# Kernel tuning notes

Hardware: AMD Instinct MI355X
Metric: run time of the kernel (lower is better)

## Reference

```python
import jax, jax.numpy as jnp
import numpy as np

N, DIM, HEADS, DH, WS = 32768, 1024, 8, 64, 256
INNER = HEADS * DH
MASK_VAL = -1e10  # ATTN_MASK_VALUE
EPS = 1e-5


def setup_inputs() -> dict:
    key = jax.random.key(0)
    k0, k1, k2 = jax.random.split(key, 3)
    x = jax.random.normal(k0, (N, DIM), jnp.float32)
    # rotary sin/cos with interleaved-pair layout matching rotate_every_two
    inv_freq = 1.0 / (10000.0 ** (jnp.arange(0, DH, 2, dtype=jnp.float32) / DH))
    freqs = jnp.arange(N, dtype=jnp.float32)[:, None] * inv_freq[None, :]  # [N, DH/2]
    sin = jnp.repeat(jnp.sin(freqs), 2, axis=-1)  # [N, DH]
    cos = jnp.repeat(jnp.cos(freqs), 2, axis=-1)  # [N, DH]
    gamma = jnp.ones((DIM,), jnp.float32)
    beta = jnp.zeros((DIM,), jnp.float32)
    w_qkv = jax.random.normal(k1, (DIM, 3 * INNER), jnp.float32) * 0.02
    w_out = jax.random.normal(k2, (INNER, DIM), jnp.float32) * 0.02
    b_out = jnp.zeros((DIM,), jnp.float32)
    return dict(x=x, sin=sin, cos=cos, gamma=gamma, beta=beta,
                w_qkv=w_qkv, w_out=w_out, b_out=b_out)


def _rotate_every_two(t):
    t1, t2 = t[..., 0::2], t[..., 1::2]
    return jnp.stack((-t2, t1), axis=-1).reshape(t.shape)


def _apply_rotary(t, sin, cos):
    # rot_dim == DH (full rotary), so no pass-through slice needed
    return t * cos + _rotate_every_two(t) * sin


def reference(x, sin, cos, gamma, beta, w_qkv, w_out, b_out):
    # LayerNorm (elementwise affine)
    mu = jnp.mean(x, axis=-1, keepdims=True)
    var = jnp.var(x, axis=-1, keepdims=True)
    x = (x - mu) * jax.lax.rsqrt(var + EPS) * gamma + beta
    # token shift: shift first half of channels by one token
    half = DIM // 2
    x_shift = jnp.pad(x[:, :half], ((1, 0), (0, 0)))[:-1]
    x = jnp.concatenate([x_shift, x[:, half:]], axis=-1)
    # qkv projection (no bias)
    qkv = x @ w_qkv  # [N, 3*INNER]
    q, k, v = jnp.split(qkv, 3, axis=-1)
    to_heads = lambda t: t.reshape(N, HEADS, DH).transpose(1, 0, 2)  # [H, N, DH]
    q, k, v = to_heads(q), to_heads(k), to_heads(v)
    # inline rotary on q, k AND v (as in source)
    q = _apply_rotary(q, sin, cos)
    k = _apply_rotary(k, sin, cos)
    v = _apply_rotary(v, sin, cos)
    # window split: [H, w, WS, DH]
    w = N // WS
    q, k, v = (t.reshape(HEADS, w, WS, DH) for t in (q, k, v))
    # look-back: each window attends to (previous window ++ current window)
    def lookback(t):
        t = jnp.pad(t, ((0, 0), (1, 0), (0, 0), (0, 0)))  # zero window at front
        return jnp.concatenate([t[:, :-1], t[:, 1:]], axis=2)  # [H, w, 2*WS, DH]
    k, v = lookback(k), lookback(v)
    sim = jnp.einsum('hwid,hwjd->hwij', q, k) * (DH ** -0.5)  # [H, w, WS, 2*WS]
    mask = jnp.tril(jnp.ones((WS, 2 * WS), dtype=bool), k=WS)  # j <= i + WS (causal)
    sim = jnp.where(mask, sim, MASK_VAL)
    attn = jax.nn.softmax(sim, axis=-1)
    out = jnp.einsum('hwij,hwjd->hwid', attn, v)  # [H, w, WS, DH]
    out = out.transpose(1, 2, 0, 3).reshape(N, INNER)  # '(w n) (h d)'
    return out @ w_out + b_out
```

## Files before the change

kernel.cpp:

```cpp
#include <hip/hip_runtime.h>

typedef __attribute__((ext_vector_type(4))) unsigned short us4;
typedef __attribute__((ext_vector_type(8))) unsigned short us8;
typedef __attribute__((ext_vector_type(8))) short s8;
typedef __attribute__((ext_vector_type(4))) float f32x4;
typedef __attribute__((ext_vector_type(16))) float f32x16;

#define NTOK 32768
#define DIM_ 1024
#define HEADS_ 8
#define DH_ 64
#define WS_ 256
#define NWIN_ 128
#define INNER_ 512

__device__ __forceinline__ float b2f(unsigned short u) {
  union { unsigned u; float f; } x; x.u = ((unsigned)u) << 16; return x.f;
}
__device__ __forceinline__ unsigned short f2b(float f) {
  union { float f; unsigned u; } x; x.f = f;
  unsigned r = x.u + 0x7FFFu + ((x.u >> 16) & 1u);
  return (unsigned short)(r >> 16);
}
__device__ __forceinline__ unsigned pk2(float a, float b) {
  return (unsigned)f2b(a) | ((unsigned)f2b(b) << 16);
}
__device__ __forceinline__ s8 mk_s8(unsigned w0, unsigned w1, unsigned w2, unsigned w3) {
  union { unsigned u[4]; s8 v; } x;
  x.u[0] = w0; x.u[1] = w1; x.u[2] = w2; x.u[3] = w3;
  return x.v;
}

__device__ __forceinline__ void gload_lds16(const unsigned short* g, void* l) {
  __builtin_amdgcn_global_load_lds((const __attribute__((address_space(1))) void*)g,
                                   (__attribute__((address_space(3))) void*)l, 16, 0, 0);
}

__global__ __launch_bounds__(256) void ln_shift(const float* __restrict__ x,
                                                const float* __restrict__ gamma,
                                                const float* __restrict__ beta,
                                                unsigned short* __restrict__ xs) {
  int row = blockIdx.x;
  int t = threadIdx.x;
  f32x4 v = ((const f32x4*)(x + (size_t)row * DIM_))[t];
  float sum = 0.f, ss = 0.f;
#pragma unroll
  for (int j = 0; j < 4; j++) { sum += v[j]; ss += v[j] * v[j]; }
#pragma unroll
  for (int off = 32; off >= 1; off >>= 1) {
    sum += __shfl_xor(sum, off);
    ss  += __shfl_xor(ss, off);
  }
  __shared__ float red[2][4];
  int wave = t >> 6, l = t & 63;
  if (l == 0) { red[0][wave] = sum; red[1][wave] = ss; }
  __syncthreads();
  sum = red[0][0] + red[0][1] + red[0][2] + red[0][3];
  ss  = red[1][0] + red[1][1] + red[1][2] + red[1][3];
  float mu = sum * (1.0f / DIM_);
  float var = ss * (1.0f / DIM_) - mu * mu;
  float rs = rsqrtf(var + 1e-5f);
  f32x4 g = ((const f32x4*)gamma)[t];
  f32x4 bb = ((const f32x4*)beta)[t];
  us4 o;
#pragma unroll
  for (int j = 0; j < 4; j++) o[j] = f2b((v[j] - mu) * rs * g[j] + bb[j]);
  int c0 = t * 4;
  if (c0 >= 512) {
    *(us4*)(xs + (size_t)row * DIM_ + c0) = o;
  } else {
    if (row + 1 < NTOK) *(us4*)(xs + (size_t)(row + 1) * DIM_ + c0) = o;
    if (row == 0) { us4 z = {0, 0, 0, 0}; *(us4*)(xs + c0) = z; }
  }
}

__global__ __launch_bounds__(256) void transpose_f32_bf16(const float* __restrict__ in,
                                                          unsigned short* __restrict__ out,
                                                          int R, int C) {
  __shared__ unsigned short tile[32][33];
  int bx = blockIdx.x * 32, by = blockIdx.y * 32;
  int tx = threadIdx.x, ty = threadIdx.y;
#pragma unroll
  for (int i = 0; i < 32; i += 8) tile[ty + i][tx] = f2b(in[(size_t)(by + ty + i) * C + bx + tx]);
  __syncthreads();
#pragma unroll
  for (int i = 0; i < 32; i += 8) out[(size_t)(bx + ty + i) * R + by + tx] = tile[tx][ty + i];
}

template <int MODE>
__global__ __launch_bounds__(512, 2) void gemm_p12(const unsigned short* __restrict__ A,
                                                   const unsigned short* __restrict__ Bt,
                                                   void* __restrict__ Cv,
                                                   const float* __restrict__ bias,
                                                   const float* __restrict__ sinp,
                                                   const float* __restrict__ cosp,
                                                   unsigned short* __restrict__ qh,
                                                   unsigned short* __restrict__ kh,
                                                   unsigned short* __restrict__ vt,
                                                   int M, int N, int K) {
  __shared__ __align__(16) char lds[163840];
  int t = threadIdx.x;
  int l = t & 63, lg = l >> 4, ll = l & 15;
  int wave = t >> 6;
  int wm = wave >> 2, wn = wave & 3;

  int nbx = gridDim.x;
  int nwg = nbx * gridDim.y;
  int flat = blockIdx.y * nbx + blockIdx.x;
  int swz = (flat & 7) * (nwg >> 3) + (flat >> 3);
  int m0 = (swz / nbx) * 256, n0 = (swz % nbx) * 256;

  const f32x4 fz = {0.f, 0.f, 0.f, 0.f};
  f32x4 acc[8][4];
#pragma unroll
  for (int m = 0; m < 8; m++)
#pragma unroll
    for (int n = 0; n < 4; n++) acc[m][n] = fz;

  int srow = t >> 3;
  int sunit = (t & 7) ^ (srow & 7);
  const unsigned short* gA = A + (size_t)(m0 + srow) * K + sunit * 8;
  const unsigned short* gB = Bt + (size_t)(n0 + srow) * K + sunit * 8;
  int t16 = t * 16;
  int nk = K >> 6;

#pragma unroll
  for (int j = 0; j < 4; j++) gload_lds16(gA + (size_t)(j * 64) * K, lds + j * 8192 + t16);
#pragma unroll
  for (int j = 0; j < 4; j++) gload_lds16(gB + (size_t)(j * 64) * K, lds + 98304 + j * 8192 + t16);
#pragma unroll
  for (int j = 0; j < 4; j++) gload_lds16(gA + 64 + (size_t)(j * 64) * K, lds + 32768 + j * 8192 + t16);
  asm volatile("s_waitcnt vmcnt(4)" ::: "memory");
  __builtin_amdgcn_sched_barrier(0);
  __builtin_amdgcn_s_barrier();

  for (int kt = 0; kt < nk; ++kt) {
    const char* sa = lds + (kt % 3) * 32768;
    const char* sb = lds + 98304 + (kt & 1) * 32768;
    s8 bf[4];
#pragma unroll
    for (int p = 0; p < 4; ++p) {
      const int qm = p & 1, kk = p >> 1;
      __builtin_amdgcn_sched_barrier(0);
      s8 af[4];
#pragma unroll
      for (int m = 0; m < 4; m++) {
        int r = wm * 128 + qm * 64 + m * 16 + ll;
        af[m] = *(const s8*)(sa + r * 128 + (((kk * 4 + lg) ^ (r & 7)) << 4));
      }
      if (qm == 0) {
#pragma unroll
        for (int n = 0; n < 4; n++) {
          int r = wn * 64 + n * 16 + ll;
          bf[n] = *(const s8*)(sb + r * 128 + (((kk * 4 + lg) ^ (r & 7)) << 4));
        }
      }
      if (p == 0 && kt + 1 < nk) {
        const unsigned short* nB = gB + (kt + 1) * 64;
        char* dB = lds + 98304 + ((kt + 1) & 1) * 32768;
#pragma unroll
        for (int j = 0; j < 4; j++) gload_lds16(nB + (size_t)(j * 64) * K, dB + j * 8192 + t16);
      }
      if (p == 1 && kt + 2 < nk) {
        const unsigned short* nA = gA + (kt + 2) * 64;
        char* dA = lds + ((kt + 2) % 3) * 32768;
#pragma unroll
        for (int j = 0; j < 4; j++) gload_lds16(nA + (size_t)(j * 64) * K, dA + j * 8192 + t16);
      }
      __builtin_amdgcn_sched_barrier(0);
      __builtin_amdgcn_s_barrier();
      __builtin_amdgcn_sched_barrier(0);
      __builtin_amdgcn_s_setprio(1);
#pragma unroll
      for (int m = 0; m < 4; m++)
#pragma unroll
        for (int n = 0; n < 4; n++)
          acc[qm * 4 + m][n] =
              __builtin_amdgcn_mfma_f32_16x16x32_bf16(af[m], bf[n], acc[qm * 4 + m][n], 0, 0, 0);
      __builtin_amdgcn_s_setprio(0);
      if (p == 3) {
        if (kt < nk - 2)       asm volatile("s_waitcnt vmcnt(4)" ::: "memory");
        else if (kt == nk - 2) asm volatile("s_waitcnt vmcnt(0)" ::: "memory");
      }
      __builtin_amdgcn_sched_barrier(0);
      __builtin_amdgcn_s_barrier();
    }
  }

  if (MODE == 0) {
    int third = n0 >> 9;
    if (third == 2) {
      bool odd = (ll & 1) != 0;
#pragma unroll
      for (int m = 0; m < 8; m++) {
        int row0 = m0 + wm * 128 + m * 16 + lg * 4;
#pragma unroll
        for (int n = 0; n < 4; n++) {
          int cit = (n0 - 1024) + wn * 64 + n * 16 + ll;
          int head = cit >> 6, d = cit & 63;
          us4 st;
#pragma unroll
          for (int r = 0; r < 4; r++) {
            float v = acc[m][n][r];
            float p = __shfl_xor(v, 1);
            float sn = sinp[(size_t)(row0 + r) * 64 + d];
            float cs = cosp[(size_t)(row0 + r) * 64 + d];
            st[r] = f2b(odd ? (v * cs + p * sn) : (v * cs - p * sn));
          }
          *(us4*)(vt + ((size_t)head * 64 + d) * NTOK + row0) = st;
        }
      }
    } else {
      int b = ll & 3, q = ll >> 2;
      bool bo1 = (b & 1) != 0, bo2 = (b & 2) != 0;
#pragma unroll
      for (int m = 0; m < 8; m++) {
        int row = m0 + wm * 128 + m * 16 + lg * 4 + b;
#pragma unroll
        for (int n = 0; n < 4; n++) {
          float v0 = acc[m][n][0], v1 = acc[m][n][1], v2 = acc[m][n][2], v3 = acc[m][n][3];
          float x0 = __shfl_xor(v1, 1);
          float x1 = __shfl_xor(v0, 1);
          float x2 = __shfl_xor(v3, 1);
          float x3 = __shfl_xor(v2, 1);
          float u0 = bo1 ? x0 : v0;
          float u1 = bo1 ? v1 : x1;
          float u2 = bo1 ? x2 : v2;
          float u3 = bo1 ? v3 : x3;
          float y0 = __shfl_xor(u2, 2);
          float y1 = __shfl_xor(u3, 2);
          float y2 = __shfl_xor(u0, 2);
          float y3 = __shfl_xor(u1, 2);
          float w0 = bo2 ? y0 : u0;
          float w1 = bo2 ? y1 : u1;
          float w2 = bo2 ? u2 : y2;
          float w3 = bo2 ? u3 : y3;
          int cb = n0 + wn * 64 + n * 16 + q * 4;
          int cit = cb & 511;
          int head = cit >> 6, d0 = cit & 63;
          f32x4 s4 = *(const f32x4*)(sinp + (size_t)row * 64 + d0);
          f32x4 c4 = *(const f32x4*)(cosp + (size_t)row * 64 + d0);
          us4 st;
          st[0] = f2b(w0 * c4[0] - w1 * s4[0]);
          st[1] = f2b(w1 * c4[1] + w0 * s4[1]);
          st[2] = f2b(w2 * c4[2] - w3 * s4[2]);
          st[3] = f2b(w3 * c4[3] + w2 * s4[3]);
          if (third == 0) *(us4*)(qh + ((size_t)head * NTOK + row) * 64 + d0) = st;
          else            *(us4*)(kh + ((size_t)head * NTOK + row) * 64 + d0) = st;
        }
      }
    }
  } else {
#pragma unroll
    for (int n = 0; n < 4; n++) {
      int col = n0 + wn * 64 + n * 16 + ll;
      float bs = bias ? bias[col] : 0.0f;
#pragma unroll
      for (int m = 0; m < 8; m++) {
#pragma unroll
        for (int r = 0; r < 4; r++) {
          int row = m0 + wm * 128 + m * 16 + lg * 4 + r;
          ((float*)Cv)[(size_t)row * N + col] = acc[m][n][r] + bs;
        }
      }
    }
  }
}

__global__ __launch_bounds__(256, 4) void attn_kernel(const unsigned short* __restrict__ qh,
                                                      const unsigned short* __restrict__ kh,
                                                      const unsigned short* __restrict__ vt,
                                                      unsigned short* __restrict__ ao) {
  __shared__ char kbuf[2][8192];
  __shared__ char vbuf[8192];
  int half = blockIdx.x, w = blockIdx.y, h = blockIdx.z;
  int t = threadIdx.x;
  int wave = t >> 6, l = t & 63;
  int l31 = l & 31, hi = l >> 5;
  const unsigned short* qb = qh + (size_t)h * NTOK * 64;
  const unsigned short* kb = kh + (size_t)h * NTOK * 64;
  const unsigned short* vb = vt + (size_t)h * 64 * NTOK;

  int qw = half * 128 + wave * 32 + l31;
  int qn = w * 256 + qw;
  s8 qf[4];
#pragma unroll
  for (int dht = 0; dht < 4; dht++)
    qf[dht] = *(const s8*)(qb + (size_t)qn * 64 + dht * 16 + hi * 8);

  f32x16 o0 = {}, o1 = {};
  float dsum = (w == 0) ? 128.f : 0.f;
  int n0 = w * 256 - 256;
  int c0 = (w == 0) ? 4 : 0;

  int srow = wave * 16 + (l >> 3);
  int sunit = l & 7;

  {
    const unsigned short* g = kb + (size_t)(n0 + c0 * 64 + srow) * 64 + ((sunit ^ (srow & 7)) * 8);
    gload_lds16(g, kbuf[c0 & 1] + wave * 2048);
    gload_lds16(g + 8 * 64, kbuf[c0 & 1] + wave * 2048 + 1024);
  }
  __syncthreads();

  for (int c = c0; c < 8; ++c) {
    int cb = n0 + c * 64;
    {
      int d = srow;
      const unsigned short* g = vb + (size_t)d * NTOK + cb + ((sunit ^ (d & 7)) * 8);
      gload_lds16(g, vbuf + wave * 2048);
      gload_lds16(g + (size_t)8 * NTOK, vbuf + wave * 2048 + 1024);
    }
    if (c < 7) {
      const unsigned short* g = kb + (size_t)(cb + 64 + srow) * 64 + ((sunit ^ (srow & 7)) * 8);
      gload_lds16(g, kbuf[(c + 1) & 1] + wave * 2048);
      gload_lds16(g + 8 * 64, kbuf[(c + 1) & 1] + wave * 2048 + 1024);
    }

    f32x16 s[2] = {{}, {}};
    const char* kl = kbuf[c & 1];
#pragma unroll
    for (int kt = 0; kt < 2; kt++) {
#pragma unroll
      for (int dht = 0; dht < 4; dht++) {
        int row = kt * 32 + l31;
        int unit = (dht * 2 + hi) ^ (row & 7);
        s8 kf = *(const s8*)(kl + row * 128 + unit * 16);
        s[kt] = __builtin_amdgcn_mfma_f32_32x32x16_bf16(kf, qf[dht], s[kt], 0, 0, 0);
      }
    }

    unsigned P0[2][4], P1[2][4];
#pragma unroll
    for (int kt = 0; kt < 2; kt++) {
#pragma unroll
      for (int r = 0; r < 16; r++) {
        int j = c * 64 + kt * 32 + (r & 3) + 8 * (r >> 2) + hi * 4;
        float e = (j <= qw + 256) ? __expf(s[kt][r] * 0.125f) : 0.f;
        s[kt][r] = e;
        dsum += e;
      }
#pragma unroll
      for (int j2 = 0; j2 < 4; j2++) {
        P0[kt][j2] = pk2(s[kt][j2 * 4 + 0], s[kt][j2 * 4 + 1]);
        P1[kt][j2] = pk2(s[kt][j2 * 4 + 2], s[kt][j2 * 4 + 3]);
      }
    }

    __syncthreads();

#pragma unroll
    for (int tt = 0; tt < 4; tt++) {
      int kt = tt >> 1, ss = tt & 1;
      unsigned a = P0[kt][2 * ss], b = P1[kt][2 * ss];
      unsigned cx = P0[kt][2 * ss + 1], dx = P1[kt][2 * ss + 1];
      asm volatile("v_permlane32_swap_b32 %0, %1" : "+v"(a), "+v"(cx));
      asm volatile("v_permlane32_swap_b32 %0, %1" : "+v"(b), "+v"(dx));
      s8 pf = mk_s8(a, b, cx, dx);
      {
        int row = l31;
        int unit = (tt * 2 + hi) ^ (row & 7);
        s8 vf = *(const s8*)(vbuf + row * 128 + unit * 16);
        o0 = __builtin_amdgcn_mfma_f32_32x32x16_bf16(vf, pf, o0, 0, 0, 0);
      }
      {
        int row = 32 + l31;
        int unit = (tt * 2 + hi) ^ (row & 7);
        s8 vf = *(const s8*)(vbuf + row * 128 + unit * 16);
        o1 = __builtin_amdgcn_mfma_f32_32x32x16_bf16(vf, pf, o1, 0, 0, 0);
      }
    }
    __syncthreads();
  }

  dsum += __shfl_xor(dsum, 32);
  float inv = 1.f / dsum;

  unsigned short* orow = ao + (size_t)qn * INNER_ + h * 64;
#pragma unroll
  for (int g = 0; g < 4; g++) {
    us4 st0, st1;
#pragma unroll
    for (int rr = 0; rr < 4; rr++) {
      st0[rr] = f2b(o0[g * 4 + rr] * inv);
      st1[rr] = f2b(o1[g * 4 + rr] * inv);
    }
    *(us4*)(orow + g * 8 + hi * 4) = st0;
    *(us4*)(orow + 32 + g * 8 + hi * 4) = st1;
  }
}

extern "C" void kernel_launch(void* const* d_in, const int* in_sizes, int n_in,
                              void* d_out, int out_size, void* d_ws, size_t ws_size,
                              hipStream_t stream) {
  const float* x     = (const float*)d_in[0];
  const float* sin_  = (const float*)d_in[1];
  const float* cos_  = (const float*)d_in[2];
  const float* gamma = (const float*)d_in[3];
  const float* beta  = (const float*)d_in[4];
  const float* w_qkv = (const float*)d_in[5];
  const float* w_out = (const float*)d_in[6];
  const float* b_out = (const float*)d_in[7];

  char* ws = (char*)d_ws;
  const size_t OFF_WQT = 0;
  const size_t OFF_WOT = 3145728;
  const size_t OFF_XS  = 4194304;
  const size_t OFF_QH  = 71303168;
  const size_t OFF_KH  = 104857600;
  const size_t OFF_VT  = 138412032;
  const size_t NEEDED  = 171966464;
  if (ws_size < NEEDED) return;

  unsigned short* wqT = (unsigned short*)(ws + OFF_WQT);
  unsigned short* woT = (unsigned short*)(ws + OFF_WOT);
  unsigned short* xs  = (unsigned short*)(ws + OFF_XS);
  unsigned short* qh  = (unsigned short*)(ws + OFF_QH);
  unsigned short* kh  = (unsigned short*)(ws + OFF_KH);
  unsigned short* vt  = (unsigned short*)(ws + OFF_VT);
  unsigned short* ao  = xs;

  transpose_f32_bf16<<<dim3(1536 / 32, 1024 / 32), dim3(32, 8), 0, stream>>>(w_qkv, wqT, 1024, 1536);
  transpose_f32_bf16<<<dim3(1024 / 32, 512 / 32), dim3(32, 8), 0, stream>>>(w_out, woT, 512, 1024);
  ln_shift<<<NTOK, 256, 0, stream>>>(x, gamma, beta, xs);
  gemm_p12<0><<<dim3(1536 / 256, NTOK / 256), 512, 0, stream>>>(
      xs, wqT, nullptr, nullptr, sin_, cos_, qh, kh, vt, NTOK, 1536, 1024);
  attn_kernel<<<dim3(2, NWIN_, HEADS_), 256, 0, stream>>>(qh, kh, vt, ao);
  gemm_p12<1><<<dim3(1024 / 256, NTOK / 256), 512, 0, stream>>>(
      ao, woT, (void*)d_out, b_out, nullptr, nullptr, nullptr, nullptr, nullptr, NTOK, 1024, 512);
}
```

Before: 334.0 us.

## Load GEMM B operand directly into registers, double-buffer A in LDS

Reworks the bf16 GEMM main loop so the weight (B) fragments are loaded from global memory straight into registers with register double-buffering, instead of staging them through LDS. The A tile uses a two-stage LDS double buffer in place of the previous three-stage one, which cuts LDS to 64 KB and the number of barriers per k-step. The trade-off is more VGPR use for the B fragments, direct global loads per wave that may be less coalesced and are duplicated across waves sharing wn, and a full vmcnt(0) wait at the end of each k-step, which may expose load latency.

```diff
diff --git a/kernel.cpp b/kernel.cpp
--- a/kernel.cpp
+++ b/kernel.cpp
@@ -87,8 +87,56 @@
   for (int i = 0; i < 32; i += 8) out[(size_t)(bx + ty + i) * R + by + tx] = tile[tx][ty + i];
 }
 
+__device__ __forceinline__ void gemm_tile_body(int kt, int nk, char* lds,
+                                               const unsigned short* gA,
+                                               const unsigned short* gB0,
+                                               const unsigned short* gB1,
+                                               const unsigned short* gB2,
+                                               const unsigned short* gB3,
+                                               int K, int t16,
+                                               f32x4 (&acc)[8][4],
+                                               s8 (&bu)[8], s8 (&bn)[8],
+                                               int wm, int ll, int lg) {
+  const char* sa = lds + (kt & 1) * 32768;
+  __builtin_amdgcn_sched_barrier(0);
+  if (kt + 1 < nk) {
+    char* dA = lds + ((kt + 1) & 1) * 32768;
+    const unsigned short* nA = gA + (kt + 1) * 64;
+#pragma unroll
+    for (int j = 0; j < 4; j++) gload_lds16(nA + (size_t)(j * 64) * K, dA + j * 8192 + t16);
+    int c = (kt + 1) * 64;
+    bn[0] = *(const s8*)(gB0 + c);  bn[4] = *(const s8*)(gB0 + c + 32);
+    bn[1] = *(const s8*)(gB1 + c);  bn[5] = *(const s8*)(gB1 + c + 32);
+    bn[2] = *(const s8*)(gB2 + c);  bn[6] = *(const s8*)(gB2 + c + 32);
+    bn[3] = *(const s8*)(gB3 + c);  bn[7] = *(const s8*)(gB3 + c + 32);
+  }
+  __builtin_amdgcn_sched_barrier(0);
+#pragma unroll
+  for (int p = 0; p < 4; ++p) {
+    const int qm = p & 1, kk = p >> 1;
+    s8 af[4];
+#pragma unroll
+    for (int m = 0; m < 4; m++) {
+      int r = wm * 128 + qm * 64 + m * 16 + ll;
+      af[m] = *(const s8*)(sa + r * 128 + (((kk * 4 + lg) ^ (r & 7)) << 4));
+    }
+    __builtin_amdgcn_s_setprio(1);
+#pragma unroll
+    for (int m = 0; m < 4; m++)
+#pragma unroll
+      for (int n = 0; n < 4; n++)
+        acc[qm * 4 + m][n] =
+            __builtin_amdgcn_mfma_f32_16x16x32_bf16(af[m], bu[kk * 4 + n], acc[qm * 4 + m][n], 0, 0, 0);
+    __builtin_amdgcn_s_setprio(0);
+  }
+  if (kt + 1 < nk) asm volatile("s_waitcnt vmcnt(0)" ::: "memory");
+  __builtin_amdgcn_sched_barrier(0);
+  __builtin_amdgcn_s_barrier();
+  __builtin_amdgcn_sched_barrier(0);
+}
+
 template <int MODE>
-__global__ __launch_bounds__(512, 2) void gemm_p12(const unsigned short* __restrict__ A,
+__global__ __launch_bounds__(512, 2) void gemm_p13(const unsigned short* __restrict__ A,
                                                    const unsigned short* __restrict__ Bt,
                                                    void* __restrict__ Cv,
                                                    const float* __restrict__ bias,
@@ -98,7 +146,7 @@
                                                    unsigned short* __restrict__ kh,
                                                    unsigned short* __restrict__ vt,
                                                    int M, int N, int K) {
-  __shared__ __align__(16) char lds[163840];
+  __shared__ __align__(16) char lds[65536];
   int t = threadIdx.x;
   int l = t & 63, lg = l >> 4, ll = l & 15;
   int wave = t >> 6;
@@ -120,71 +168,30 @@
   int srow = t >> 3;
   int sunit = (t & 7) ^ (srow & 7);
   const unsigned short* gA = A + (size_t)(m0 + srow) * K + sunit * 8;
-  const unsigned short* gB = Bt + (size_t)(n0 + srow) * K + sunit * 8;
   int t16 = t * 16;
   int nk = K >> 6;
 
+  const unsigned short* gB0 = Bt + (size_t)(n0 + wn * 64 + ll) * K + lg * 8;
+  const unsigned short* gB1 = gB0 + (size_t)16 * K;
+  const unsigned short* gB2 = gB0 + (size_t)32 * K;
+  const unsigned short* gB3 = gB0 + (size_t)48 * K;
+
+  s8 b0[8], b1[8];
+
 #pragma unroll
   for (int j = 0; j < 4; j++) gload_lds16(gA + (size_t)(j * 64) * K, lds + j * 8192 + t16);
-#pragma unroll
-  for (int j = 0; j < 4; j++) gload_lds16(gB + (size_t)(j * 64) * K, lds + 98304 + j * 8192 + t16);
-#pragma unroll
-  for (int j = 0; j < 4; j++) gload_lds16(gA + 64 + (size_t)(j * 64) * K, lds + 32768 + j * 8192 + t16);
-  asm volatile("s_waitcnt vmcnt(4)" ::: "memory");
+  b0[0] = *(const s8*)(gB0);  b0[4] = *(const s8*)(gB0 + 32);
+  b0[1] = *(const s8*)(gB1);  b0[5] = *(const s8*)(gB1 + 32);
+  b0[2] = *(const s8*)(gB2);  b0[6] = *(const s8*)(gB2 + 32);
+  b0[3] = *(const s8*)(gB3);  b0[7] = *(const s8*)(gB3 + 32);
+  asm volatile("s_waitcnt vmcnt(0)" ::: "memory");
   __builtin_amdgcn_sched_barrier(0);
   __builtin_amdgcn_s_barrier();
-
-  for (int kt = 0; kt < nk; ++kt) {
-    const char* sa = lds + (kt % 3) * 32768;
-    const char* sb = lds + 98304 + (kt & 1) * 32768;
-    s8 bf[4];
-#pragma unroll
-    for (int p = 0; p < 4; ++p) {
-      const int qm = p & 1, kk = p >> 1;
-      __builtin_amdgcn_sched_barrier(0);
-      s8 af[4];
-#pragma unroll
-      for (int m = 0; m < 4; m++) {
-        int r = wm * 128 + qm * 64 + m * 16 + ll;
-        af[m] = *(const s8*)(sa + r * 128 + (((kk * 4 + lg) ^ (r & 7)) << 4));
-      }
-      if (qm == 0) {
-#pragma unroll
-        for (int n = 0; n < 4; n++) {
-          int r = wn * 64 + n * 16 + ll;
-          bf[n] = *(const s8*)(sb + r * 128 + (((kk * 4 + lg) ^ (r & 7)) << 4));
-        }
-      }
-      if (p == 0 && kt + 1 < nk) {
-        const unsigned short* nB = gB + (kt + 1) * 64;
-        char* dB = lds + 98304 + ((kt + 1) & 1) * 32768;
-#pragma unroll
-        for (int j = 0; j < 4; j++) gload_lds16(nB + (size_t)(j * 64) * K, dB + j * 8192 + t16);
-      }
-      if (p == 1 && kt + 2 < nk) {
-        const unsigned short* nA = gA + (kt + 2) * 64;
-        char* dA = lds + ((kt + 2) % 3) * 32768;
-#pragma unroll
-        for (int j = 0; j < 4; j++) gload_lds16(nA + (size_t)(j * 64) * K, dA + j * 8192 + t16);
-      }
-      __builtin_amdgcn_sched_barrier(0);
-      __builtin_amdgcn_s_barrier();
-      __builtin_amdgcn_sched_barrier(0);
-      __builtin_amdgcn_s_setprio(1);
-#pragma unroll
-      for (int m = 0; m < 4; m++)
-#pragma unroll
-        for (int n = 0; n < 4; n++)
-          acc[qm * 4 + m][n] =
-              __builtin_amdgcn_mfma_f32_16x16x32_bf16(af[m], bf[n], acc[qm * 4 + m][n], 0, 0, 0);
-      __builtin_amdgcn_s_setprio(0);
-      if (p == 3) {
-        if (kt < nk - 2)       asm volatile("s_waitcnt vmcnt(4)" ::: "memory");
-        else if (kt == nk - 2) asm volatile("s_waitcnt vmcnt(0)" ::: "memory");
-      }
-      __builtin_amdgcn_sched_barrier(0);
-      __builtin_amdgcn_s_barrier();
-    }
+  __builtin_amdgcn_sched_barrier(0);
+
+  for (int kt2 = 0; kt2 < nk; kt2 += 2) {
+    gemm_tile_body(kt2, nk, lds, gA, gB0, gB1, gB2, gB3, K, t16, acc, b0, b1, wm, ll, lg);
+    gemm_tile_body(kt2 + 1, nk, lds, gA, gB0, gB1, gB2, gB3, K, t16, acc, b1, b0, wm, ll, lg);
   }
 
   if (MODE == 0) {
@@ -423,9 +430,9 @@
   transpose_f32_bf16<<<dim3(1536 / 32, 1024 / 32), dim3(32, 8), 0, stream>>>(w_qkv, wqT, 1024, 1536);
   transpose_f32_bf16<<<dim3(1024 / 32, 512 / 32), dim3(32, 8), 0, stream>>>(w_out, woT, 512, 1024);
   ln_shift<<<NTOK, 256, 0, stream>>>(x, gamma, beta, xs);
-  gemm_p12<0><<<dim3(1536 / 256, NTOK / 256), 512, 0, stream>>>(
+  gemm_p13<0><<<dim3(1536 / 256, NTOK / 256), 512, 0, stream>>>(
       xs, wqT, nullptr, nullptr, sin_, cos_, qh, kh, vt, NTOK, 1536, 1024);
   attn_kernel<<<dim3(2, NWIN_, HEADS_), 256, 0, stream>>>(qh, kh, vt, ao);
-  gemm_p12<1><<<dim3(1024 / 256, NTOK / 256), 512, 0, stream>>>(
+  gemm_p13<1><<<dim3(1024 / 256, NTOK / 256), 512, 0, stream>>>(
       ao, woT, (void*)d_out, b_out, nullptr, nullptr, nullptr, nullptr, nullptr, NTOK, 1024, 512);
 }
```

New measurement: 490.8 us, median of 2. 1.47x slower.
